# Performance work log

Hardware: AMD Instinct MI355X
Metric: run time of the kernel (lower is better)

Reference implementation:

```python
import jax, jax.numpy as jnp
import numpy as np
from jax import lax

EPS = 1e-5


def _bn_eval(x, gamma, beta, mean, var, axis=1):
    # eval-mode batchnorm over channel axis
    shape = [1] * x.ndim
    shape[axis] = -1
    g = gamma.reshape(shape); b = beta.reshape(shape)
    m = mean.reshape(shape); v = var.reshape(shape)
    return (x - m) * (g * lax.rsqrt(v + EPS)) + b


def setup_inputs() -> dict:
    key = jax.random.key(0)
    ks = jax.random.split(key, 12)
    B, C, H, W, K = 16, 256, 128, 128, 5
    x_feat = jax.random.normal(ks[0], (B, C, H, W), jnp.float32)
    raw_img = jax.random.uniform(ks[1], (B, 3, H, W), jnp.float32)
    # img_feature: Conv2d(3,64,3,pad=1) + BN(64)
    w_conv1 = jax.random.normal(ks[2], (64, 3, 3, 3), jnp.float32) * 0.1
    b_conv1 = jax.random.normal(ks[3], (64,), jnp.float32) * 0.1
    g1 = jnp.ones((64,), jnp.float32)
    beta1 = jnp.zeros((64,), jnp.float32)
    m1 = jax.random.normal(ks[4], (64,), jnp.float32) * 0.1
    v1 = jax.random.uniform(ks[5], (64,), jnp.float32) + 0.5
    # conv_filter: Conv2d(64, C*K*K, 1) + BN(C*K*K)
    CK2 = C * K * K
    w_filt = jax.random.normal(ks[6], (CK2, 64), jnp.float32) * 0.05
    b_filt = jax.random.normal(ks[7], (CK2,), jnp.float32) * 0.05
    g2 = jnp.ones((CK2,), jnp.float32)
    beta2 = jnp.zeros((CK2,), jnp.float32)
    m2 = jax.random.normal(ks[8], (CK2,), jnp.float32) * 0.1
    v2 = jax.random.uniform(ks[9], (CK2,), jnp.float32) + 0.5
    return {"x_feat": x_feat, "raw_img": raw_img,
            "w_conv1": w_conv1, "b_conv1": b_conv1, "g1": g1, "beta1": beta1, "m1": m1, "v1": v1,
            "w_filt": w_filt, "b_filt": b_filt, "g2": g2, "beta2": beta2, "m2": m2, "v2": v2}


def reference(x_feat, raw_img, w_conv1, b_conv1, g1, beta1, m1, v1,
              w_filt, b_filt, g2, beta2, m2, v2):
    B, C, H, W = x_feat.shape
    K = int(round(np.sqrt(w_filt.shape[0] // C)))  # kernel_size
    pad = K // 2

    # ---- filter generation branch ----
    # Conv2d(3,64,3,pad=1)
    y = lax.conv_general_dilated(raw_img, w_conv1, (1, 1), ((1, 1), (1, 1)),
                                 dimension_numbers=("NCHW", "OIHW", "NCHW"))
    y = y + b_conv1[None, :, None, None]
    y = jax.nn.relu(_bn_eval(y, g1, beta1, m1, v1))
    img_feat = jnp.mean(y, axis=(2, 3))                        # (B, 64) global avg pool

    # 1x1 conv == dense: (B, C*K*K)
    df = img_feat @ w_filt.T + b_filt
    df = _bn_eval(df[:, :, None, None], g2, beta2, m2, v2)[:, :, 0, 0]
    df = df.reshape(B, C, K * K)
    # NOTE: original applies Softmax(dim=1) -> over the CHANNEL axis
    df = jax.nn.softmax(df, axis=1)                            # (B, C, K*K)

    # ---- per-sample dynamic depthwise conv ----
    x_pad = jnp.pad(x_feat, ((0, 0), (0, 0), (pad, pad), (pad, pad)), mode="reflect")
    filt = df.reshape(B, C, K, K)

    def dw(x, w):  # x: (C, Hp, Wp), w: (C, K, K)
        return lax.conv_general_dilated(
            x[None], w[:, None], (1, 1), "VALID",
            dimension_numbers=("NCHW", "OIHW", "NCHW"),
            feature_group_count=C)[0]

    out = jax.vmap(dw)(x_pad, filt)                            # (B, C, H, W)
    return out
```

## Files before the change

kernel.cpp:

```cpp
#include <hip/hip_runtime.h>

#define EPSV 1e-5f

typedef float f4 __attribute__((ext_vector_type(4)));
typedef float f2 __attribute__((ext_vector_type(2)));

#define B   16
#define CIN 3
#define C1  64
#define C   256
#define H   128
#define W   128
#define K   5
#define KK  25
#define FSTR 28

#define R1   8
#define WS1  32
#define TW1  36

__global__ __launch_bounds__(128) void k1_conv_pool(
    const float* __restrict__ raw, const float* __restrict__ wconv,
    const float* __restrict__ bconv, const float* __restrict__ g1,
    const float* __restrict__ be1, const float* __restrict__ m1,
    const float* __restrict__ v1, float* __restrict__ partial)
{
  const int bid   = blockIdx.x;
  const int b     = bid >> 6;
  const int chunk = (bid >> 2) & 15;
  const int wh    = bid & 3;
  const int tid   = threadIdx.x;

  __shared__ __align__(16) float t[CIN][R1 + 2][TW1];
  const float* rawb = raw + (size_t)b * CIN * H * W;
  for (int i = tid; i < CIN * (R1 + 2) * 34; i += 128) {
    int ic  = i / ((R1 + 2) * 34);
    int rem = i - ic * (R1 + 2) * 34;
    int r   = rem / 34;
    int cc  = rem - r * 34;
    int gr  = chunk * R1 + r - 1;
    int gc  = wh * WS1 + cc - 1;
    float val = 0.f;
    if ((unsigned)gr < H && (unsigned)gc < W)
      val = rawb[ic * H * W + gr * W + gc];
    t[ic][r][cc] = val;
  }
  __syncthreads();

  const int rp  = tid >> 5;
  const int grp = tid & 31;
  float wt[2][27], A[2], Bc[2];
#pragma unroll
  for (int g = 0; g < 2; ++g) {
    int c = grp * 2 + g;
#pragma unroll
    for (int k = 0; k < 27; ++k) wt[g][k] = wconv[c * 27 + k];
    float sc = g1[c] * rsqrtf(v1[c] + EPSV);
    A[g]  = sc;
    Bc[g] = (bconv[c] - m1[c]) * sc + be1[c];
  }

  f4 cur[CIN][4], nxt[CIN][4];
#pragma unroll
  for (int ic = 0; ic < CIN; ++ic)
#pragma unroll
    for (int r = 0; r < 4; ++r) cur[ic][r] = *(const f4*)&t[ic][2 * rp + r][0];

  float acc0 = 0.f, acc1 = 0.f;
#pragma unroll
  for (int j = 0; j < 8; ++j) {
#pragma unroll
    for (int ic = 0; ic < CIN; ++ic)
#pragma unroll
      for (int r = 0; r < 4; ++r) nxt[ic][r] = *(const f4*)&t[ic][2 * rp + r][4 * j + 4];

    float v[2][2][4];
#pragma unroll
    for (int q = 0; q < 2; ++q)
#pragma unroll
      for (int g = 0; g < 2; ++g)
#pragma unroll
        for (int p = 0; p < 4; ++p) v[q][g][p] = 0.f;

#pragma unroll
    for (int ic = 0; ic < CIN; ++ic) {
#pragma unroll
      for (int q = 0; q < 2; ++q) {
#pragma unroll
        for (int kh = 0; kh < 3; ++kh) {
          f4 a  = cur[ic][q + kh];
          f4 bb = nxt[ic][q + kh];
#pragma unroll
          for (int p = 0; p < 4; ++p) {
#pragma unroll
            for (int kw = 0; kw < 3; ++kw) {
              float e = (p + kw < 4) ? a[p + kw] : bb[p + kw - 4];
              v[q][0][p] += e * wt[0][ic * 9 + kh * 3 + kw];
              v[q][1][p] += e * wt[1][ic * 9 + kh * 3 + kw];
            }
          }
        }
      }
    }
#pragma unroll
    for (int q = 0; q < 2; ++q)
#pragma unroll
      for (int p = 0; p < 4; ++p) {
        acc0 += fmaxf(v[q][0][p] * A[0] + Bc[0], 0.f);
        acc1 += fmaxf(v[q][1][p] * A[1] + Bc[1], 0.f);
      }
#pragma unroll
    for (int ic = 0; ic < CIN; ++ic)
#pragma unroll
      for (int r = 0; r < 4; ++r) cur[ic][r] = nxt[ic][r];
  }

  __shared__ float red[4][C1];
  red[rp][grp * 2]     = acc0;
  red[rp][grp * 2 + 1] = acc1;
  __syncthreads();
  if (tid < C1) {
    float s = red[0][tid] + red[1][tid] + red[2][tid] + red[3][tid];
    partial[((size_t)((b * 16 + chunk) * 4 + wh)) * C1 + tid] = s;
  }
}

#define NCH 64

__global__ __launch_bounds__(256) void k2_filter(
    const float* __restrict__ partial, const float* __restrict__ wf,
    const float* __restrict__ bf, const float* __restrict__ g2,
    const float* __restrict__ be2, const float* __restrict__ m2,
    const float* __restrict__ v2, float* __restrict__ filt)
{
  const int b  = blockIdx.x / KK;
  const int kk = blockIdx.x - b * KK;
  const int c  = threadIdx.x;

  __shared__ float feat[C1];
  if (c < C1) {
    float s = 0.f;
#pragma unroll
    for (int ch = 0; ch < NCH; ++ch)
      s += partial[((size_t)b * NCH + ch) * C1 + c];
    feat[c] = s * (1.f / (H * W));
  }
  __syncthreads();

  const int idx = c * KK + kk;
  float v = bf[idx];
  const float* wr = wf + (size_t)idx * C1;
#pragma unroll
  for (int j = 0; j < C1; ++j) v += feat[j] * wr[j];
  v = (v - m2[idx]) * (g2[idx] * rsqrtf(v2[idx] + EPSV)) + be2[idx];

  __shared__ float red[256];
  red[c] = v;
  __syncthreads();
#pragma unroll
  for (int s = 128; s > 0; s >>= 1) {
    if (c < s) red[c] = fmaxf(red[c], red[c + s]);
    __syncthreads();
  }
  float mx = red[0];
  __syncthreads();
  float e = expf(v - mx);
  red[c] = e;
  __syncthreads();
#pragma unroll
  for (int s = 128; s > 0; s >>= 1) {
    if (c < s) red[c] += red[c + s];
    __syncthreads();
  }
  filt[((size_t)b * C + c) * FSTR + kk] = e / red[0];
}

#define R3  64
#define TW3 132
#define TH3 (R3 + 4)

__global__ __launch_bounds__(512) void k3_dwconv(
    const float* __restrict__ x, const float* __restrict__ filt,
    float* __restrict__ out)
{
  const int bid = blockIdx.x;
  const int swz = (bid & 7) * 1024 + (bid >> 3);
  const int plane = swz >> 1;
  const int tile  = swz & 1;
  const int r0    = tile * R3;
  const int tid   = threadIdx.x;

  const float* xp = x + (size_t)plane * H * W;
  float* op       = out + (size_t)plane * H * W;
  const float* fp = filt + (size_t)plane * FSTR;

  f4 fv[7];
#pragma unroll
  for (int i = 0; i < 7; ++i) fv[i] = *(const f4*)&fp[i << 2];

  __shared__ __align__(16) float t[TH3][TW3];

#pragma unroll
  for (int idx = tid; idx < TH3 * 32; idx += 512) {
    int r = idx >> 5, g = idx & 31;
    int gr = r0 + r - 2;
    gr = gr < 0 ? -gr : (gr >= H ? 2 * H - 2 - gr : gr);
    f4 v = *(const f4*)&xp[gr * W + (g << 2)];
    f2 lo = {v[0], v[1]};
    f2 hi = {v[2], v[3]};
    *(f2*)&t[r][(g << 2) + 2] = lo;
    *(f2*)&t[r][(g << 2) + 4] = hi;
  }
  if (tid < TH3 * 4) {
    int r = tid >> 2, c = tid & 3;
    int cc = (c == 0) ? 0 : (c == 1) ? 1 : (c == 2) ? 130 : 131;
    int gc = (c == 0) ? 2 : (c == 1) ? 1 : (c == 2) ? 126 : 125;
    int gr = r0 + r - 2;
    gr = gr < 0 ? -gr : (gr >= H ? 2 * H - 2 - gr : gr);
    t[r][cc] = xp[gr * W + gc];
  }
  __syncthreads();

  const int g  = tid & 31, w = g << 2;
  const int rb = (tid >> 5) << 2;
  f4 acc[4];
#pragma unroll
  for (int q = 0; q < 4; ++q) acc[q] = (f4){0.f, 0.f, 0.f, 0.f};

#pragma unroll
  for (int tr = 0; tr < 8; ++tr) {
    f4 a  = *(const f4*)&t[rb + tr][w];
    f4 bb = *(const f4*)&t[rb + tr][w + 4];
#pragma unroll
    for (int q = 0; q < 4; ++q) {
      if (tr - q < 0 || tr - q > 4) continue;
      const int ki = tr - q;
#pragma unroll
      for (int p = 0; p < 4; ++p) {
#pragma unroll
        for (int j = 0; j < 5; ++j) {
          float e = (p + j < 4) ? a[p + j] : bb[p + j - 4];
          const int k = ki * 5 + j;
          acc[q][p] += e * fv[k >> 2][k & 3];
        }
      }
    }
  }
#pragma unroll
  for (int q = 0; q < 4; ++q)
    __builtin_nontemporal_store(acc[q], (f4*)&op[(r0 + rb + q) * W + w]);
}

extern "C" void kernel_launch(void* const* d_in, const int* in_sizes, int n_in,
                              void* d_out, int out_size, void* d_ws, size_t ws_size,
                              hipStream_t stream) {
  const float* x_feat = (const float*)d_in[0];
  const float* raw    = (const float*)d_in[1];
  const float* wconv  = (const float*)d_in[2];
  const float* bconv  = (const float*)d_in[3];
  const float* g1     = (const float*)d_in[4];
  const float* be1    = (const float*)d_in[5];
  const float* m1     = (const float*)d_in[6];
  const float* v1     = (const float*)d_in[7];
  const float* wf     = (const float*)d_in[8];
  const float* bf     = (const float*)d_in[9];
  const float* g2     = (const float*)d_in[10];
  const float* be2    = (const float*)d_in[11];
  const float* m2     = (const float*)d_in[12];
  const float* v2     = (const float*)d_in[13];
  float* out = (float*)d_out;

  float* partial = (float*)d_ws;
  float* filt    = partial + B * NCH * C1;

  k1_conv_pool<<<B * 16 * 4, 128, 0, stream>>>(raw, wconv, bconv, g1, be1, m1, v1, partial);
  k2_filter  <<<B * KK, 256, 0, stream>>>(partial, wf, bf, g2, be2, m2, v2, filt);
  k3_dwconv  <<<B * C * (H / R3), 512, 0, stream>>>(x_feat, filt, out);
}
```

Baseline: 128.8 us.

## Software-pipeline depthwise conv over four sub-tiles with double-buffered shared memory

The depthwise conv kernel now has each block handle two full channel planes as four 64-row sub-tiles, instead of one half-plane per block. Global loads for the next sub-tile are staged in registers while the current sub-tile is computed from a double-buffered shared tile. The aim is to hide global-load latency behind compute and cut block-launch overhead. In exchange the grid is four times smaller, and shared memory and register use per block go up, which may lower occupancy.

```diff
diff --git a/kernel.cpp b/kernel.cpp
--- a/kernel.cpp
+++ b/kernel.cpp
@@ -175,80 +175,120 @@
   filt[((size_t)b * C + c) * FSTR + kk] = e / red[0];
 }
 
-#define R3  64
+#define THS 68
 #define TW3 132
-#define TH3 (R3 + 4)
+
+#define LOADSUB(xpq, r0q)                                                     \
+  {                                                                           \
+    _Pragma("unroll") for (int k = 0; k < 5; ++k) {                           \
+      int idx = tid + (k << 9);                                               \
+      if (k < 4 || tid < 128) {                                               \
+        int r = idx >> 5, g = idx & 31;                                       \
+        int gr = (r0q) + r - 2;                                               \
+        gr = gr < 0 ? -gr : (gr >= H ? 2 * H - 2 - gr : gr);                  \
+        stg[k] = *(const f4*)&(xpq)[gr * W + (g << 2)];                       \
+      }                                                                       \
+    }                                                                         \
+    if (tid < THS * 4) {                                                      \
+      int r = tid >> 2, c = tid & 3;                                          \
+      int gc = (c == 0) ? 2 : (c == 1) ? 1 : (c == 2) ? 126 : 125;            \
+      int gr = (r0q) + r - 2;                                                 \
+      gr = gr < 0 ? -gr : (gr >= H ? 2 * H - 2 - gr : gr);                    \
+      hstg = (xpq)[gr * W + gc];                                              \
+    }                                                                         \
+  }
+
+#define WRITESUB(bufi)                                                        \
+  {                                                                           \
+    _Pragma("unroll") for (int k = 0; k < 5; ++k) {                           \
+      int idx = tid + (k << 9);                                               \
+      if (k < 4 || tid < 128) {                                               \
+        int r = idx >> 5, g = idx & 31;                                       \
+        f2 lo = {stg[k][0], stg[k][1]};                                       \
+        f2 hi = {stg[k][2], stg[k][3]};                                       \
+        *(f2*)&t[bufi][r][(g << 2) + 2] = lo;                                 \
+        *(f2*)&t[bufi][r][(g << 2) + 4] = hi;                                 \
+      }                                                                       \
+    }                                                                         \
+    if (tid < THS * 4) {                                                      \
+      int r = tid >> 2, c = tid & 3;                                          \
+      int cc = (c == 0) ? 0 : (c == 1) ? 1 : (c == 2) ? 130 : 131;            \
+      t[bufi][r][cc] = hstg;                                                  \
+    }                                                                         \
+  }
+
+#define COMPUTE(bufi, opq, r0q, FV)                                           \
+  {                                                                           \
+    const int w  = (tid & 31) << 2;                                           \
+    const int rb = (tid >> 5) << 2;                                           \
+    f4 acc[4];                                                                \
+    _Pragma("unroll") for (int q = 0; q < 4; ++q)                             \
+      acc[q] = (f4){0.f, 0.f, 0.f, 0.f};                                      \
+    _Pragma("unroll") for (int tr = 0; tr < 8; ++tr) {                        \
+      f4 a  = *(const f4*)&t[bufi][rb + tr][w];                               \
+      f4 bb = *(const f4*)&t[bufi][rb + tr][w + 4];                           \
+      _Pragma("unroll") for (int q = 0; q < 4; ++q) {                         \
+        if (tr - q < 0 || tr - q > 4) continue;                               \
+        const int ki = tr - q;                                                \
+        _Pragma("unroll") for (int p = 0; p < 4; ++p) {                       \
+          _Pragma("unroll") for (int j = 0; j < 5; ++j) {                     \
+            float e = (p + j < 4) ? a[p + j] : bb[p + j - 4];                 \
+            const int kq = ki * 5 + j;                                        \
+            acc[q][p] += e * FV[kq >> 2][kq & 3];                             \
+          }                                                                   \
+        }                                                                     \
+      }                                                                       \
+    }                                                                         \
+    _Pragma("unroll") for (int q = 0; q < 4; ++q)                             \
+      __builtin_nontemporal_store(acc[q],                                     \
+          (f4*)&(opq)[((r0q) + rb + q) * W + w]);                             \
+  }
 
 __global__ __launch_bounds__(512) void k3_dwconv(
     const float* __restrict__ x, const float* __restrict__ filt,
     float* __restrict__ out)
 {
   const int bid = blockIdx.x;
-  const int swz = (bid & 7) * 1024 + (bid >> 3);
-  const int plane = swz >> 1;
-  const int tile  = swz & 1;
-  const int r0    = tile * R3;
-  const int tid   = threadIdx.x;
-
-  const float* xp = x + (size_t)plane * H * W;
-  float* op       = out + (size_t)plane * H * W;
-  const float* fp = filt + (size_t)plane * FSTR;
-
-  f4 fv[7];
-#pragma unroll
-  for (int i = 0; i < 7; ++i) fv[i] = *(const f4*)&fp[i << 2];
-
-  __shared__ __align__(16) float t[TH3][TW3];
-
-#pragma unroll
-  for (int idx = tid; idx < TH3 * 32; idx += 512) {
-    int r = idx >> 5, g = idx & 31;
-    int gr = r0 + r - 2;
-    gr = gr < 0 ? -gr : (gr >= H ? 2 * H - 2 - gr : gr);
-    f4 v = *(const f4*)&xp[gr * W + (g << 2)];
-    f2 lo = {v[0], v[1]};
-    f2 hi = {v[2], v[3]};
-    *(f2*)&t[r][(g << 2) + 2] = lo;
-    *(f2*)&t[r][(g << 2) + 4] = hi;
-  }
-  if (tid < TH3 * 4) {
-    int r = tid >> 2, c = tid & 3;
-    int cc = (c == 0) ? 0 : (c == 1) ? 1 : (c == 2) ? 130 : 131;
-    int gc = (c == 0) ? 2 : (c == 1) ? 1 : (c == 2) ? 126 : 125;
-    int gr = r0 + r - 2;
-    gr = gr < 0 ? -gr : (gr >= H ? 2 * H - 2 - gr : gr);
-    t[r][cc] = xp[gr * W + gc];
-  }
-  __syncthreads();
-
-  const int g  = tid & 31, w = g << 2;
-  const int rb = (tid >> 5) << 2;
-  f4 acc[4];
-#pragma unroll
-  for (int q = 0; q < 4; ++q) acc[q] = (f4){0.f, 0.f, 0.f, 0.f};
-
-#pragma unroll
-  for (int tr = 0; tr < 8; ++tr) {
-    f4 a  = *(const f4*)&t[rb + tr][w];
-    f4 bb = *(const f4*)&t[rb + tr][w + 4];
-#pragma unroll
-    for (int q = 0; q < 4; ++q) {
-      if (tr - q < 0 || tr - q > 4) continue;
-      const int ki = tr - q;
-#pragma unroll
-      for (int p = 0; p < 4; ++p) {
-#pragma unroll
-        for (int j = 0; j < 5; ++j) {
-          float e = (p + j < 4) ? a[p + j] : bb[p + j - 4];
-          const int k = ki * 5 + j;
-          acc[q][p] += e * fv[k >> 2][k & 3];
-        }
-      }
-    }
-  }
-#pragma unroll
-  for (int q = 0; q < 4; ++q)
-    __builtin_nontemporal_store(acc[q], (f4*)&op[(r0 + rb + q) * W + w]);
+  const int swz = (bid & 7) * 256 + (bid >> 3);
+  const int pl0 = swz << 1;
+  const int tid = threadIdx.x;
+
+  const float* xp0 = x   + (size_t)pl0 * H * W;
+  const float* xp1 = xp0 + H * W;
+  float*       op0 = out + (size_t)pl0 * H * W;
+  float*       op1 = op0 + H * W;
+  const float* fp0 = filt + (size_t)pl0 * FSTR;
+  const float* fp1 = fp0 + FSTR;
+
+  __shared__ __align__(16) float t[2][THS][TW3];
+
+  f4 stg[5]; float hstg = 0.f;
+  f4 fvA[7], fvB[7];
+#pragma unroll
+  for (int i = 0; i < 7; ++i) fvA[i] = *(const f4*)&fp0[i << 2];
+
+  LOADSUB(xp0, 0)
+  WRITESUB(0)
+  __syncthreads();
+
+  LOADSUB(xp0, 64)
+  COMPUTE(0, op0, 0, fvA)
+  WRITESUB(1)
+  __syncthreads();
+
+  LOADSUB(xp1, 0)
+#pragma unroll
+  for (int i = 0; i < 7; ++i) fvB[i] = *(const f4*)&fp1[i << 2];
+  COMPUTE(1, op0, 64, fvA)
+  WRITESUB(0)
+  __syncthreads();
+
+  LOADSUB(xp1, 64)
+  COMPUTE(0, op1, 0, fvB)
+  WRITESUB(1)
+  __syncthreads();
+
+  COMPUTE(1, op1, 64, fvB)
 }
 
 extern "C" void kernel_launch(void* const* d_in, const int* in_sizes, int n_in,
@@ -275,5 +315,5 @@
 
   k1_conv_pool<<<B * 16 * 4, 128, 0, stream>>>(raw, wconv, bconv, g1, be1, m1, v1, partial);
   k2_filter  <<<B * KK, 256, 0, stream>>>(partial, wf, bf, g2, be2, m2, v2, filt);
-  k3_dwconv  <<<B * C * (H / R3), 512, 0, stream>>>(x_feat, filt, out);
+  k3_dwconv  <<<B * C / 2, 512, 0, stream>>>(x_feat, filt, out);
 }
```

Result: faster. 123.5 us (-4.2%).
